# Performance work log

Hardware: AMD Instinct MI355X
Metric: run time of the kernel (lower is better)

Reference implementation:

```python
import jax, jax.numpy as jnp
import numpy as np

# RReLU in eval mode == leaky relu with slope (lower+upper)/2
_SLOPE = (0.001 + 0.004) / 2.0  # 0.0025

def _rrelu(x):
    return jnp.where(x >= 0, x, _SLOPE * x)

_DIMS = [(8, 8), (8, 4), (4, 4), (4, 4), (4, 4), (4, 4), (4, 1),
         (1, 4), (4, 4), (4, 4), (4, 4), (4, 4), (4, 8)]
_NAMES = ['in', 'h1', 'h2', 'h3', 'h4', 'h5', 'encode',
          'h6', 'h7', 'h8', 'h9', 'h10', 'decode']


def setup_inputs() -> dict:
    key = jax.random.key(0)
    keys = jax.random.split(key, 1 + 2 * len(_DIMS))
    inp = {'x_in': jax.random.normal(keys[0], (4194304, 8), dtype=jnp.float32)}
    for i, (name, (fi, fo)) in enumerate(zip(_NAMES, _DIMS)):
        bound = 1.0 / np.sqrt(fi)
        inp[f'W_{name}'] = jax.random.uniform(keys[1 + 2 * i], (fi, fo),
                                              minval=-bound, maxval=bound,
                                              dtype=jnp.float32)
        inp[f'b_{name}'] = jax.random.uniform(keys[2 + 2 * i], (fo,),
                                              minval=-bound, maxval=bound,
                                              dtype=jnp.float32)
    return inp


def reference(x_in, W_in, b_in, W_h1, b_h1, W_h2, b_h2, W_h3, b_h3,
              W_h4, b_h4, W_h5, b_h5, W_encode, b_encode, W_h6, b_h6,
              W_h7, b_h7, W_h8, b_h8, W_h9, b_h9, W_h10, b_h10,
              W_decode, b_decode):
    lin = lambda x, W, b: x @ W + b
    x = x_in  # (x - mean)/std with mean=0, std=1 is identity
    x = lin(_rrelu(lin(x, W_in, b_in)), W_h1, b_h1)
    x = x + lin(_rrelu(lin(x, W_h2, b_h2)), W_h3, b_h3)
    x = x + lin(_rrelu(lin(x, W_h4, b_h4)), W_h5, b_h5)
    x_encode = _rrelu(lin(x, W_encode, b_encode))
    x = _rrelu(lin(x_encode, W_h6, b_h6))
    x = x + lin(_rrelu(lin(x, W_h7, b_h7)), W_h8, b_h8)
    x = x + lin(_rrelu(lin(x, W_h9, b_h9)), W_h10, b_h10)
    x_decode = _rrelu(lin(x, W_decode, b_decode))
    return (x_encode, x_decode)
```

## Files before the change

### kernel.cpp

```cpp
#include <hip/hip_runtime.h>

#define N_ROWS 4194304
#define RPT 8
#define BLOCK 256

enum : int {
    O_W_in = 0,    O_b_in = 64,
    O_W_h1 = 72,   O_b_h1 = 104,
    O_W_h2 = 108,  O_b_h2 = 124,
    O_W_h3 = 128,  O_b_h3 = 144,
    O_W_h4 = 148,  O_b_h4 = 164,
    O_W_h5 = 168,  O_b_h5 = 184,
    O_W_enc = 188, O_b_enc = 192,
    O_W_h6 = 196,  O_b_h6 = 200,
    O_W_h7 = 204,  O_b_h7 = 220,
    O_W_h8 = 224,  O_b_h8 = 240,
    O_W_h9 = 244,  O_b_h9 = 260,
    O_W_h10 = 264, O_b_h10 = 280,
    O_W_dec = 284, O_b_dec = 316,
    W_TOTAL = 324
};

__device__ __forceinline__ float rrelu(float v) {
    return fmaxf(v, 0.0025f * v);
}

template <int FI, int FO, bool RELU>
__device__ __forceinline__ void lin(const float* ws, int Woff, int boff,
                                    const float (&x)[RPT][FI],
                                    float (&y)[RPT][FO]) {
#pragma unroll
    for (int jg = 0; jg < FO; jg += 4) {
        float4 b4 = *reinterpret_cast<const float4*>(ws + boff + jg);
        float acc[RPT][4];
#pragma unroll
        for (int k = 0; k < RPT; ++k) {
            acc[k][0] = b4.x; acc[k][1] = b4.y;
            acc[k][2] = b4.z; acc[k][3] = b4.w;
        }
#pragma unroll
        for (int i = 0; i < FI; ++i) {
            float4 w4 = *reinterpret_cast<const float4*>(ws + Woff + i * FO + jg);
            float wa[4] = {w4.x, w4.y, w4.z, w4.w};
#pragma unroll
            for (int k = 0; k < RPT; ++k)
#pragma unroll
                for (int c = 0; c < 4; ++c)
                    acc[k][c] = fmaf(x[k][i], wa[c], acc[k][c]);
        }
#pragma unroll
        for (int k = 0; k < RPT; ++k)
#pragma unroll
            for (int c = 0; c < 4; ++c)
                y[k][jg + c] = RELU ? rrelu(acc[k][c]) : acc[k][c];
    }
}

template <int FI, int FO>
__device__ __forceinline__ void lin_add(const float* ws, int Woff, int boff,
                                        const float (&x)[RPT][FI],
                                        float (&y)[RPT][FO]) {
#pragma unroll
    for (int jg = 0; jg < FO; jg += 4) {
        float4 b4 = *reinterpret_cast<const float4*>(ws + boff + jg);
        float acc[RPT][4];
#pragma unroll
        for (int k = 0; k < RPT; ++k) {
            acc[k][0] = b4.x; acc[k][1] = b4.y;
            acc[k][2] = b4.z; acc[k][3] = b4.w;
        }
#pragma unroll
        for (int i = 0; i < FI; ++i) {
            float4 w4 = *reinterpret_cast<const float4*>(ws + Woff + i * FO + jg);
            float wa[4] = {w4.x, w4.y, w4.z, w4.w};
#pragma unroll
            for (int k = 0; k < RPT; ++k)
#pragma unroll
                for (int c = 0; c < 4; ++c)
                    acc[k][c] = fmaf(x[k][i], wa[c], acc[k][c]);
        }
#pragma unroll
        for (int k = 0; k < RPT; ++k)
#pragma unroll
            for (int c = 0; c < 4; ++c) y[k][jg + c] += acc[k][c];
    }
}

__device__ __forceinline__ void resblock(const float* ws, int Oa, int Oba,
                                         int Ob, int Obb, float (&x)[RPT][4]) {
    float t[RPT][4];
    lin<4, 4, true>(ws, Oa, Oba, x, t);
    lin_add<4, 4>(ws, Ob, Obb, t, x);
}

__global__ __launch_bounds__(BLOCK) void ann_fused_kernel(
    const float* __restrict__ x_in, const float* __restrict__ wf,
    float* __restrict__ out) {
    __shared__ float ws[W_TOTAL];
    {
        const int t = threadIdx.x;
        if (t < W_TOTAL) ws[t] = wf[t];
        if (t + BLOCK < W_TOTAL) ws[t + BLOCK] = wf[t + BLOCK];
        __syncthreads();
    }

    const int tid = blockIdx.x * BLOCK + threadIdx.x;
    const int T = N_ROWS / RPT;

    float xin[RPT][8];
#pragma unroll
    for (int k = 0; k < RPT; ++k) {
        const float4* p =
            reinterpret_cast<const float4*>(x_in + (size_t)(tid + k * T) * 8);
        float4 a = p[0], b = p[1];
        xin[k][0] = a.x; xin[k][1] = a.y; xin[k][2] = a.z; xin[k][3] = a.w;
        xin[k][4] = b.x; xin[k][5] = b.y; xin[k][6] = b.z; xin[k][7] = b.w;
    }

    float t8[RPT][8];
    lin<8, 8, true>(ws, O_W_in, O_b_in, xin, t8);
    float x[RPT][4];
    lin<8, 4, false>(ws, O_W_h1, O_b_h1, t8, x);

    resblock(ws, O_W_h2, O_b_h2, O_W_h3, O_b_h3, x);
    resblock(ws, O_W_h4, O_b_h4, O_W_h5, O_b_h5, x);

    float4 we = *reinterpret_cast<const float4*>(ws + O_W_enc);
    float be = ws[O_b_enc];
    float e[RPT];
#pragma unroll
    for (int k = 0; k < RPT; ++k) {
        float a = fmaf(x[k][0], we.x, be);
        a = fmaf(x[k][1], we.y, a);
        a = fmaf(x[k][2], we.z, a);
        a = fmaf(x[k][3], we.w, a);
        e[k] = rrelu(a);
    }

    float4 w6 = *reinterpret_cast<const float4*>(ws + O_W_h6);
    float4 b6 = *reinterpret_cast<const float4*>(ws + O_b_h6);
#pragma unroll
    for (int k = 0; k < RPT; ++k) {
        x[k][0] = rrelu(fmaf(e[k], w6.x, b6.x));
        x[k][1] = rrelu(fmaf(e[k], w6.y, b6.y));
        x[k][2] = rrelu(fmaf(e[k], w6.z, b6.z));
        x[k][3] = rrelu(fmaf(e[k], w6.w, b6.w));
    }

    resblock(ws, O_W_h7, O_b_h7, O_W_h8, O_b_h8, x);
    resblock(ws, O_W_h9, O_b_h9, O_W_h10, O_b_h10, x);

    float d[RPT][8];
    lin<4, 8, true>(ws, O_W_dec, O_b_dec, x, d);

#pragma unroll
    for (int k = 0; k < RPT; ++k) {
        const int row = tid + k * T;
        out[row] = e[k];
        float4* q = reinterpret_cast<float4*>(out + N_ROWS + (size_t)row * 8);
        q[0] = make_float4(d[k][0], d[k][1], d[k][2], d[k][3]);
        q[1] = make_float4(d[k][4], d[k][5], d[k][6], d[k][7]);
    }
}

struct SrcPtrs { const float* p[26]; };

__global__ void pack_weights(SrcPtrs s, float* __restrict__ wf) {
    const int t = threadIdx.x;
    const int off[26] = {O_W_in,  O_b_in,  O_W_h1,  O_b_h1,  O_W_h2, O_b_h2,
                         O_W_h3,  O_b_h3,  O_W_h4,  O_b_h4,  O_W_h5, O_b_h5,
                         O_W_enc, O_b_enc, O_W_h6,  O_b_h6,  O_W_h7, O_b_h7,
                         O_W_h8,  O_b_h8,  O_W_h9,  O_b_h9,  O_W_h10,
                         O_b_h10, O_W_dec, O_b_dec};
    const int sz[26] = {64, 8, 32, 4, 16, 4, 16, 4, 16, 4, 16, 4, 4,
                        1,  4, 4,  16, 4, 16, 4, 16, 4, 16, 4, 32, 8};
#pragma unroll 1
    for (int g = 0; g < 26; ++g)
        if (t < sz[g]) wf[off[g] + t] = s.p[g][t];
}

extern "C" void kernel_launch(void* const* d_in, const int* in_sizes, int n_in,
                              void* d_out, int out_size, void* d_ws, size_t ws_size,
                              hipStream_t stream) {
    const float* x_in = (const float*)d_in[0];
    float* wf = (float*)d_ws;

    SrcPtrs s;
    for (int i = 0; i < 26; ++i) s.p[i] = (const float*)d_in[1 + i];
    pack_weights<<<1, 64, 0, stream>>>(s, wf);

    float* out = (float*)d_out;
    const int total_threads = N_ROWS / RPT;
    dim3 grid(total_threads / BLOCK), block(BLOCK);
    ann_fused_kernel<<<grid, block, 0, stream>>>(x_in, wf, out);
}
```

Baseline: 328.3 us.

## Software-pipeline input loads across two row batches per thread

Each thread still handles 8 rows, but now as two batches of 4. The next batch's input is prefetched into registers while the current batch's MLP is computed, which is meant to overlap global-load latency with compute. The lin and lin_add helpers are merged into one template with an ADD flag. The extra nxt buffer and the loop raise register pressure, and a single prefetch stage with only two iterations gives limited overlap.

After: 667.1 us. +103.2%, slower.

```diff
diff --git a/kernel.cpp b/kernel.cpp
--- a/kernel.cpp
+++ b/kernel.cpp
@@ -1,7 +1,8 @@
 #include <hip/hip_runtime.h>
 
 #define N_ROWS 4194304
-#define RPT 8
+#define RPT 4
+#define ITERS 2
 #define BLOCK 256
 
 enum : int {
@@ -25,7 +26,7 @@
     return fmaxf(v, 0.0025f * v);
 }
 
-template <int FI, int FO, bool RELU>
+template <int FI, int FO, bool RELU, bool ADD>
 __device__ __forceinline__ void lin(const float* ws, int Woff, int boff,
                                     const float (&x)[RPT][FI],
                                     float (&y)[RPT][FO]) {
@@ -51,46 +52,31 @@
 #pragma unroll
         for (int k = 0; k < RPT; ++k)
 #pragma unroll
-            for (int c = 0; c < 4; ++c)
-                y[k][jg + c] = RELU ? rrelu(acc[k][c]) : acc[k][c];
-    }
-}
-
-template <int FI, int FO>
-__device__ __forceinline__ void lin_add(const float* ws, int Woff, int boff,
-                                        const float (&x)[RPT][FI],
-                                        float (&y)[RPT][FO]) {
-#pragma unroll
-    for (int jg = 0; jg < FO; jg += 4) {
-        float4 b4 = *reinterpret_cast<const float4*>(ws + boff + jg);
-        float acc[RPT][4];
-#pragma unroll
-        for (int k = 0; k < RPT; ++k) {
-            acc[k][0] = b4.x; acc[k][1] = b4.y;
-            acc[k][2] = b4.z; acc[k][3] = b4.w;
-        }
-#pragma unroll
-        for (int i = 0; i < FI; ++i) {
-            float4 w4 = *reinterpret_cast<const float4*>(ws + Woff + i * FO + jg);
-            float wa[4] = {w4.x, w4.y, w4.z, w4.w};
-#pragma unroll
-            for (int k = 0; k < RPT; ++k)
-#pragma unroll
-                for (int c = 0; c < 4; ++c)
-                    acc[k][c] = fmaf(x[k][i], wa[c], acc[k][c]);
-        }
-#pragma unroll
-        for (int k = 0; k < RPT; ++k)
-#pragma unroll
-            for (int c = 0; c < 4; ++c) y[k][jg + c] += acc[k][c];
+            for (int c = 0; c < 4; ++c) {
+                float v = RELU ? rrelu(acc[k][c]) : acc[k][c];
+                if (ADD) y[k][jg + c] += v; else y[k][jg + c] = v;
+            }
     }
 }
 
 __device__ __forceinline__ void resblock(const float* ws, int Oa, int Oba,
                                          int Ob, int Obb, float (&x)[RPT][4]) {
     float t[RPT][4];
-    lin<4, 4, true>(ws, Oa, Oba, x, t);
-    lin_add<4, 4>(ws, Ob, Obb, t, x);
+    lin<4, 4, true, false>(ws, Oa, Oba, x, t);
+    lin<4, 4, false, true>(ws, Ob, Obb, t, x);
+}
+
+__device__ __forceinline__ void load_batch(const float* __restrict__ x_in,
+                                           unsigned tid, unsigned kbase,
+                                           unsigned T, float (&xb)[RPT][8]) {
+#pragma unroll
+    for (int k = 0; k < RPT; ++k) {
+        const float4* p = reinterpret_cast<const float4*>(
+            x_in + (size_t)(tid + (kbase + k) * T) * 8u);
+        float4 a = p[0], b = p[1];
+        xb[k][0] = a.x; xb[k][1] = a.y; xb[k][2] = a.z; xb[k][3] = a.w;
+        xb[k][4] = b.x; xb[k][5] = b.y; xb[k][6] = b.z; xb[k][7] = b.w;
+    }
 }
 
 __global__ __launch_bounds__(BLOCK) void ann_fused_kernel(
@@ -104,62 +90,68 @@
         __syncthreads();
     }
 
-    const int tid = blockIdx.x * BLOCK + threadIdx.x;
-    const int T = N_ROWS / RPT;
+    const unsigned tid = blockIdx.x * BLOCK + threadIdx.x;
+    const unsigned T = N_ROWS / (RPT * ITERS);
 
-    float xin[RPT][8];
+    float cur[RPT][8], nxt[RPT][8];
+    load_batch(x_in, tid, 0, T, cur);
+
+#pragma unroll 1
+    for (int it = 0; it < ITERS; ++it) {
+        if (it + 1 < ITERS) load_batch(x_in, tid, (it + 1) * RPT, T, nxt);
+
+        float t8[RPT][8];
+        lin<8, 8, true, false>(ws, O_W_in, O_b_in, cur, t8);
+        float x[RPT][4];
+        lin<8, 4, false, false>(ws, O_W_h1, O_b_h1, t8, x);
+
+        resblock(ws, O_W_h2, O_b_h2, O_W_h3, O_b_h3, x);
+        resblock(ws, O_W_h4, O_b_h4, O_W_h5, O_b_h5, x);
+
+        float4 we = *reinterpret_cast<const float4*>(ws + O_W_enc);
+        float be = ws[O_b_enc];
+        float e[RPT];
 #pragma unroll
-    for (int k = 0; k < RPT; ++k) {
-        const float4* p =
-            reinterpret_cast<const float4*>(x_in + (size_t)(tid + k * T) * 8);
-        float4 a = p[0], b = p[1];
-        xin[k][0] = a.x; xin[k][1] = a.y; xin[k][2] = a.z; xin[k][3] = a.w;
-        xin[k][4] = b.x; xin[k][5] = b.y; xin[k][6] = b.z; xin[k][7] = b.w;
-    }
+        for (int k = 0; k < RPT; ++k) {
+            float a = fmaf(x[k][0], we.x, be);
+            a = fmaf(x[k][1], we.y, a);
+            a = fmaf(x[k][2], we.z, a);
+            a = fmaf(x[k][3], we.w, a);
+            e[k] = rrelu(a);
+        }
 
-    float t8[RPT][8];
-    lin<8, 8, true>(ws, O_W_in, O_b_in, xin, t8);
-    float x[RPT][4];
-    lin<8, 4, false>(ws, O_W_h1, O_b_h1, t8, x);
+        float4 w6 = *reinterpret_cast<const float4*>(ws + O_W_h6);
+        float4 b6 = *reinterpret_cast<const float4*>(ws + O_b_h6);
+#pragma unroll
+        for (int k = 0; k < RPT; ++k) {
+            x[k][0] = rrelu(fmaf(e[k], w6.x, b6.x));
+            x[k][1] = rrelu(fmaf(e[k], w6.y, b6.y));
+            x[k][2] = rrelu(fmaf(e[k], w6.z, b6.z));
+            x[k][3] = rrelu(fmaf(e[k], w6.w, b6.w));
+        }
 
-    resblock(ws, O_W_h2, O_b_h2, O_W_h3, O_b_h3, x);
-    resblock(ws, O_W_h4, O_b_h4, O_W_h5, O_b_h5, x);
+        resblock(ws, O_W_h7, O_b_h7, O_W_h8, O_b_h8, x);
+        resblock(ws, O_W_h9, O_b_h9, O_W_h10, O_b_h10, x);
 
-    float4 we = *reinterpret_cast<const float4*>(ws + O_W_enc);
-    float be = ws[O_b_enc];
-    float e[RPT];
-#pragma unroll
-    for (int k = 0; k < RPT; ++k) {
-        float a = fmaf(x[k][0], we.x, be);
-        a = fmaf(x[k][1], we.y, a);
-        a = fmaf(x[k][2], we.z, a);
-        a = fmaf(x[k][3], we.w, a);
-        e[k] = rrelu(a);
-    }
-
-    float4 w6 = *reinterpret_cast<const float4*>(ws + O_W_h6);
-    float4 b6 = *reinterpret_cast<const float4*>(ws + O_b_h6);
-#pragma unroll
-    for (int k = 0; k < RPT; ++k) {
-        x[k][0] = rrelu(fmaf(e[k], w6.x, b6.x));
-        x[k][1] = rrelu(fmaf(e[k], w6.y, b6.y));
-        x[k][2] = rrelu(fmaf(e[k], w6.z, b6.z));
-        x[k][3] = rrelu(fmaf(e[k], w6.w, b6.w));
-    }
-
-    resblock(ws, O_W_h7, O_b_h7, O_W_h8, O_b_h8, x);
-    resblock(ws, O_W_h9, O_b_h9, O_W_h10, O_b_h10, x);
-
-    float d[RPT][8];
-    lin<4, 8, true>(ws, O_W_dec, O_b_dec, x, d);
+        float d[RPT][8];
+        lin<4, 8, true, false>(ws, O_W_dec, O_b_dec, x, d);
 
 #pragma unroll
-    for (int k = 0; k < RPT; ++k) {
-        const int row = tid + k * T;
-        out[row] = e[k];
-        float4* q = reinterpret_cast<float4*>(out + N_ROWS + (size_t)row * 8);
-        q[0] = make_float4(d[k][0], d[k][1], d[k][2], d[k][3]);
-        q[1] = make_float4(d[k][4], d[k][5], d[k][6], d[k][7]);
+        for (int k = 0; k < RPT; ++k) {
+            const unsigned row = tid + (it * RPT + k) * T;
+            out[row] = e[k];
+            float4* q =
+                reinterpret_cast<float4*>(out + N_ROWS + (size_t)row * 8u);
+            q[0] = make_float4(d[k][0], d[k][1], d[k][2], d[k][3]);
+            q[1] = make_float4(d[k][4], d[k][5], d[k][6], d[k][7]);
+        }
+
+        if (it + 1 < ITERS) {
+#pragma unroll
+            for (int k = 0; k < RPT; ++k)
+#pragma unroll
+                for (int i = 0; i < 8; ++i) cur[k][i] = nxt[k][i];
+        }
     }
 }
 
@@ -190,7 +182,7 @@
     pack_weights<<<1, 64, 0, stream>>>(s, wf);
 
     float* out = (float*)d_out;
-    const int total_threads = N_ROWS / RPT;
+    const int total_threads = N_ROWS / (RPT * ITERS);
     dim3 grid(total_threads / BLOCK), block(BLOCK);
     ann_fused_kernel<<<grid, block, 0, stream>>>(x_in, wf, out);
 }
```
